# Optimization experiments

Measured on AMD Instinct MI355X. Metric: run time of the kernel, lower is better.

## Reference

```python
import jax, jax.numpy as jnp
from jax import lax
import numpy as np

B, T, I, H = 512, 512, 128, 256


def setup_inputs() -> dict:
    key = jax.random.key(0)
    ks = jax.random.split(key, 7)
    s = 1.0 / np.sqrt(H)  # pytorch-style init scale
    return {
        "x": jax.random.normal(ks[0], (B, T, I), dtype=jnp.float32),
        "h0": jax.random.normal(ks[1], (1, B, H), dtype=jnp.float32),
        "c0": jax.random.normal(ks[2], (1, B, H), dtype=jnp.float32),
        "w_ih": jax.random.normal(ks[3], (4 * H, I), dtype=jnp.float32) * s,
        "w_hh": jax.random.normal(ks[4], (4 * H, H), dtype=jnp.float32) * s,
        "b_ih": jax.random.normal(ks[5], (4 * H,), dtype=jnp.float32) * s,
        "b_hh": jax.random.normal(ks[6], (4 * H,), dtype=jnp.float32) * s,
    }


def reference(x, h0, c0, w_ih, w_hh, b_ih, b_hh):
    """Single-layer LSTM; returns final cell state c_n of shape [1, B, H].
    Gate row order in w_*/b_* is PyTorch's (i, f, g, o) blocks of H."""
    h = h0[0]  # [B, H]
    c = c0[0]  # [B, H]
    # Precompute input contribution for all timesteps: [T, B, 4H]
    xg = jnp.einsum('bti,gi->tbg', x, w_ih) + (b_ih + b_hh)

    def step(carry, xg_t):
        h, c = carry
        g = xg_t + h @ w_hh.T  # [B, 4H]
        gi, gf, gg, go = jnp.split(g, 4, axis=-1)
        c_new = jax.nn.sigmoid(gf) * c + jax.nn.sigmoid(gi) * jnp.tanh(gg)
        h_new = jax.nn.sigmoid(go) * jnp.tanh(c_new)
        return (h_new, c_new), None

    (h_T, c_T), _ = lax.scan(step, (h, c), xg)
    return c_T[None]  # [1, B, H]
```

## Files before the change

kernel.cpp:

```cpp
#include <hip/hip_runtime.h>
#include <hip/hip_bf16.h>
#include <hip/hip_fp16.h>


typedef __attribute__((ext_vector_type(4))) float f32x4;
typedef __attribute__((ext_vector_type(8))) _Float16 f16x8;
typedef __attribute__((ext_vector_type(4))) unsigned int u32x4;
typedef __attribute__((ext_vector_type(4))) int i32x4;

static __device__ __forceinline__ float h2f(unsigned short u) {
  return (float)__builtin_bit_cast(_Float16, u);
}
static __device__ __forceinline__ unsigned short f2h(float f) {
  return __builtin_bit_cast(unsigned short, (_Float16)f);
}
static __device__ __forceinline__ float fast_sigmoid(float x) {
  return __builtin_amdgcn_rcpf(1.0f + __builtin_amdgcn_exp2f(-1.44269504f * x));
}
static __device__ __forceinline__ float fast_tanh(float x) {
  return 1.0f - 2.0f * __builtin_amdgcn_rcpf(1.0f + __builtin_amdgcn_exp2f(2.88539008f * x));
}

__global__ void zero2(float* p) { if (threadIdx.x < 2) p[threadIdx.x] = 0.f; }

__global__ void absmax_red(const float* __restrict__ src, int n, float* __restrict__ out) {
  __shared__ float s[256];
  float m = 0.f;
  for (int i = blockIdx.x * 256 + threadIdx.x; i < n; i += gridDim.x * 256)
    m = fmaxf(m, fabsf(src[i]));
  s[threadIdx.x] = m; __syncthreads();
  for (int w = 128; w > 0; w >>= 1) {
    if (threadIdx.x < w) s[threadIdx.x] = fmaxf(s[threadIdx.x], s[threadIdx.x + w]);
    __syncthreads();
  }
  if (threadIdx.x == 0) atomicMax((int*)out, __float_as_int(s[0]));
}

__global__ void quant_w(const float* __restrict__ w, const float* __restrict__ scales,
                        signed char* __restrict__ wq, int n) {
  int i = blockIdx.x * 256 + threadIdx.x;
  if (i < n) {
    float inv = 127.0f / scales[0];
    int q = (int)rintf(w[i] * inv);
    q = max(-127, min(127, q));
    wq[i] = (signed char)q;
  }
}

__global__ void wperm_cast(const float* __restrict__ w, unsigned short* __restrict__ dst) {
  int i = (blockIdx.x * 256 + threadIdx.x) * 4;
  if (i < 131072) {
    int q = i >> 7, k = i & 127;
    int p = (q & 3) * 256 + (q >> 2);
    f32x4 v = *(const f32x4*)(w + p * 128 + k);
    ushort4 pk;
    pk.x = f2h(v[0]); pk.y = f2h(v[1]); pk.z = f2h(v[2]); pk.w = f2h(v[3]);
    *(ushort4*)(dst + i) = pk;
  }
}

__global__ void bias_perm(const float* __restrict__ bi, const float* __restrict__ bh,
                          float* __restrict__ bc) {
  int q = blockIdx.x * 256 + threadIdx.x;
  int p = (q & 3) * 256 + (q >> 2);
  bc[q] = bi[p] + bh[p];
}

__global__ void state_init(const float* __restrict__ h0, const float* __restrict__ c0,
                           const float* __restrict__ scales,
                           signed char* __restrict__ hst, float* __restrict__ cst) {
  int i = blockIdx.x * 256 + threadIdx.x;
  float inv = 127.0f / scales[1];
  int q = (int)rintf(h0[i] * inv);
  q = max(-127, min(127, q));
  hst[i] = (signed char)q;
  cst[i] = c0[i];
}

__global__ __launch_bounds__(256) void xgemm(
    const float* __restrict__ x, const unsigned short* __restrict__ wih,
    const float* __restrict__ bconv,
    unsigned short* __restrict__ xg, int t0, int tclog) {
  __shared__ unsigned short Ash[128 * 128];
  __shared__ unsigned short Bsh[128 * 128];

  const int tid  = threadIdx.x;
  const int lane = tid & 63;
  const int wv   = tid >> 6;
  const int c16  = lane & 15;
  const int gq   = lane >> 4;
  const long m0  = (long)blockIdx.x * 128;
  const int tcm  = (1 << tclog) - 1;

#pragma unroll
  for (int i = 0; i < 16; ++i) {
    int fidx = (i * 256 + tid) * 4;
    int row = fidx >> 7, k = fidx & 127;
    long cr = m0 + row;
    long b  = cr >> tclog;
    long tl = cr & tcm;
    f32x4 v = *(const f32x4*)(x + ((size_t)b * 512 + t0 + tl) * 128 + k);
    ushort4 pk;
    pk.x = f2h(v[0]); pk.y = f2h(v[1]); pk.z = f2h(v[2]); pk.w = f2h(v[3]);
    int byte = (row * 256 + k * 2) ^ ((row & 7) << 4);
    *(ushort4*)((char*)Ash + byte) = pk;
  }

  const int mh = (wv >> 1) * 64;
  const int nh = (wv & 1) * 64;

  for (int nc = 0; nc < 8; ++nc) {
    __syncthreads();
    {
      const char* wb = (const char*)(wih + nc * 128 * 128);
#pragma unroll
      for (int i = 0; i < 8; ++i) {
        int idx16 = i * 256 + tid;
        int row = idx16 >> 4, ch = idx16 & 15;
        int srcoff = row * 256 + ((ch * 16) ^ ((row & 7) << 4));
        u32x4 v = *(const u32x4*)(wb + srcoff);
        *(u32x4*)((char*)Bsh + idx16 * 16) = v;
      }
    }
    __syncthreads();

    float bias_v[4];
#pragma unroll
    for (int nt = 0; nt < 4; ++nt)
      bias_v[nt] = bconv[nc * 128 + nh + nt * 16 + c16];

    f16x8 af[4][4], bfr[4][4];
#pragma unroll
    for (int sm = 0; sm < 4; ++sm)
#pragma unroll
      for (int kt = 0; kt < 4; ++kt) {
        int m = mh + sm * 16 + c16;
        int byte = (m * 256 + (kt * 32 + gq * 8) * 2) ^ ((m & 7) << 4);
        af[sm][kt] = __builtin_bit_cast(f16x8, *(const u32x4*)((const char*)Ash + byte));
      }
#pragma unroll
    for (int nt = 0; nt < 4; ++nt)
#pragma unroll
      for (int kt = 0; kt < 4; ++kt) {
        int n = nh + nt * 16 + c16;
        int byte = (n * 256 + (kt * 32 + gq * 8) * 2) ^ ((n & 7) << 4);
        bfr[nt][kt] = __builtin_bit_cast(f16x8, *(const u32x4*)((const char*)Bsh + byte));
      }

    f32x4 acc[4][4];
#pragma unroll
    for (int sm = 0; sm < 4; ++sm)
#pragma unroll
      for (int nt = 0; nt < 4; ++nt) { f32x4 z = {0.f, 0.f, 0.f, 0.f}; acc[sm][nt] = z; }
#pragma unroll
    for (int sm = 0; sm < 4; ++sm)
#pragma unroll
      for (int nt = 0; nt < 4; ++nt)
#pragma unroll
        for (int kt = 0; kt < 4; ++kt)
          acc[sm][nt] = __builtin_amdgcn_mfma_f32_16x16x32_f16(af[sm][kt], bfr[nt][kt], acc[sm][nt], 0, 0, 0);

#pragma unroll
    for (int sm = 0; sm < 4; ++sm)
#pragma unroll
      for (int nt = 0; nt < 4; ++nt) {
        long row = m0 + mh + sm * 16 + gq * 4;
        int gcol = nc * 128 + nh + nt * 16 + c16;
#pragma unroll
        for (int r = 0; r < 4; ++r)
          xg[(size_t)(row + r) * 1024 + gcol] = f2h(acc[sm][nt][r] + bias_v[nt]);
      }
  }
}

__global__ __launch_bounds__(512)
__attribute__((amdgpu_waves_per_eu(2, 2)))
void fused_chunk(
    const unsigned short* __restrict__ xgc, const signed char* __restrict__ wq,
    const float* __restrict__ scales, signed char* __restrict__ hst,
    float* __restrict__ cst, float* __restrict__ out, int Tc, int first, int last,
    const float* __restrict__ x, const unsigned short* __restrict__ wih,
    const float* __restrict__ bconv, unsigned short* __restrict__ xgn,
    int t0n, int tclog, int do_x) {
  __shared__ char smem[65536];

  const int tid  = threadIdx.x;
  const int lane = tid & 63;
  const int wv   = tid >> 6;
  const int c16  = lane & 15;
  const int gq   = lane >> 4;

  if (blockIdx.x < 128) {
    signed char (*hb)[1280] = (signed char (*)[1280])smem;
    const int b0 = blockIdx.x * 4;

    const int col = wv * 32 + c16;
    float cv0 = cst[(b0 + gq) * 256 + col];
    float cv1 = cst[(b0 + gq) * 256 + col + 16];

    const float sw   = scales[0] * (1.0f / 127.0f);
    const float facR = sw * (1.0f / 127.0f);
    const float fac0 = first ? sw * (scales[1] * (1.0f / 127.0f)) : facR;

    i32x4 wf[8][4];
#pragma unroll
    for (int nt = 0; nt < 8; ++nt)
#pragma unroll
      for (int kt = 0; kt < 4; ++kt) {
        int n = (nt >> 1) * 256 + wv * 32 + (nt & 1) * 16 + c16;
        wf[nt][kt] = *(const i32x4*)(wq + n * 256 + kt * 64 + gq * 16);
      }
#pragma unroll
    for (int nt = 0; nt < 8; ++nt)
#pragma unroll
      for (int kt = 0; kt < 4; ++kt)
        asm volatile("" : "+v"(wf[nt][kt]));
    asm volatile("" ::: "memory");

    for (int i = tid; i < 1024; i += 512) {
      int row = i >> 8, cc = i & 255;
      hb[0][row * 320 + cc] = hst[(b0 + row) * 256 + cc];
    }

    const char* pxp = (const char*)(xgc + ((size_t)(b0 + gq) * Tc) * 1024 + col * 4);
    ushort4 px0 = *(const ushort4*)pxp;
    ushort4 px1 = *(const ushort4*)(pxp + 128);
    pxp += 2048;

    const bool mrow = (c16 & 3) == 0;
    const int  hrow = c16 >> 2;
    i32x4 af[4];
#pragma unroll
    for (int kt = 0; kt < 4; ++kt) { i32x4 z = {0, 0, 0, 0}; af[kt] = z; }
    const i32x4 zacc = {0, 0, 0, 0};
    int q0 = 0, q1 = 0;

    __syncthreads();

    for (int tt = 0; tt < Tc; ++tt) {
      const int cur = tt & 1;

      if (mrow) {
        const signed char* hp = &hb[cur][hrow * 320 + gq * 16];
        af[0] = *(const i32x4*)(hp);
        af[1] = *(const i32x4*)(hp + 64);
        af[2] = *(const i32x4*)(hp + 128);
        af[3] = *(const i32x4*)(hp + 192);
      }

      ushort4 pn0 = *(const ushort4*)pxp;
      ushort4 pn1 = *(const ushort4*)(pxp + 128);
      pxp += 2048;

      i32x4 acc[8];
#pragma unroll
      for (int ne = 0; ne < 4; ++ne)
        acc[2 * ne] = __builtin_amdgcn_mfma_i32_16x16x64_i8(af[0], wf[2 * ne][0], zacc, 0, 0, 0);
#pragma unroll
      for (int kt = 1; kt < 4; ++kt)
#pragma unroll
        for (int ne = 0; ne < 4; ++ne)
          acc[2 * ne] = __builtin_amdgcn_mfma_i32_16x16x64_i8(af[kt], wf[2 * ne][kt], acc[2 * ne], 0, 0, 0);
#pragma unroll
      for (int ne = 0; ne < 4; ++ne)
        acc[2 * ne + 1] = __builtin_amdgcn_mfma_i32_16x16x64_i8(af[0], wf[2 * ne + 1][0], zacc, 0, 0, 0);
#pragma unroll
      for (int kt = 1; kt < 4; ++kt)
#pragma unroll
        for (int ne = 0; ne < 4; ++ne)
          acc[2 * ne + 1] = __builtin_amdgcn_mfma_i32_16x16x64_i8(af[kt], wf[2 * ne + 1][kt], acc[2 * ne + 1], 0, 0, 0);

      const float fac = (tt == 0) ? fac0 : facR;

      {
        float gi = __builtin_fmaf((float)acc[0][0], fac, h2f(px0.x));
        float gf = __builtin_fmaf((float)acc[2][0], fac, h2f(px0.y));
        float gg = __builtin_fmaf((float)acc[4][0], fac, h2f(px0.z));
        float go = __builtin_fmaf((float)acc[6][0], fac, h2f(px0.w));
        cv0 = fast_sigmoid(gf) * cv0 + fast_sigmoid(gi) * fast_tanh(gg);
        float hn = fast_sigmoid(go) * fast_tanh(cv0);
        q0 = (int)rintf(hn * 127.0f);
        hb[cur ^ 1][gq * 320 + col] = (signed char)q0;
      }
      {
        float gi = __builtin_fmaf((float)acc[1][0], fac, h2f(px1.x));
        float gf = __builtin_fmaf((float)acc[3][0], fac, h2f(px1.y));
        float gg = __builtin_fmaf((float)acc[5][0], fac, h2f(px1.z));
        float go = __builtin_fmaf((float)acc[7][0], fac, h2f(px1.w));
        cv1 = fast_sigmoid(gf) * cv1 + fast_sigmoid(gi) * fast_tanh(gg);
        float hn = fast_sigmoid(go) * fast_tanh(cv1);
        q1 = (int)rintf(hn * 127.0f);
        hb[cur ^ 1][gq * 320 + col + 16] = (signed char)q1;
      }

      px0 = pn0; px1 = pn1;
      __syncthreads();
    }

    cst[(b0 + gq) * 256 + col]      = cv0;
    cst[(b0 + gq) * 256 + col + 16] = cv1;
    hst[(b0 + gq) * 256 + col]      = (signed char)q0;
    hst[(b0 + gq) * 256 + col + 16] = (signed char)q1;
    if (last) {
      out[(b0 + gq) * 256 + col]      = cv0;
      out[(b0 + gq) * 256 + col + 16] = cv1;
    }
  } else if (do_x) {
    unsigned short* Ash = (unsigned short*)smem;
    unsigned short* Bsh = (unsigned short*)(smem + 32768);
    const int tcm    = (1 << tclog) - 1;
    const int ntiles = Tc << 2;
    const int wm = wv >> 2, wn = wv & 3;
    const int mh = wm * 64, nh = wn * 32;

    for (int rt = (int)blockIdx.x - 128; rt < ntiles; rt += 128) {
      const long m0 = (long)rt * 128;
      __syncthreads();

#pragma unroll
      for (int i = 0; i < 8; ++i) {
        int fidx = (i * 512 + tid) * 4;
        int row = fidx >> 7, k = fidx & 127;
        long cr = m0 + row;
        long b  = cr >> tclog;
        long tl = cr & tcm;
        f32x4 v = *(const f32x4*)(x + ((size_t)b * 512 + t0n + tl) * 128 + k);
        ushort4 pk;
        pk.x = f2h(v[0]); pk.y = f2h(v[1]); pk.z = f2h(v[2]); pk.w = f2h(v[3]);
        int byte = (row * 256 + k * 2) ^ ((row & 7) << 4);
        *(ushort4*)((char*)Ash + byte) = pk;
      }

      for (int nc = 0; nc < 8; ++nc) {
        __syncthreads();
        {
          const char* wb = (const char*)(wih + nc * 128 * 128);
#pragma unroll
          for (int i = 0; i < 4; ++i) {
            int idx16 = i * 512 + tid;
            int row = idx16 >> 4, ch = idx16 & 15;
            int srcoff = row * 256 + ((ch * 16) ^ ((row & 7) << 4));
            u32x4 v = *(const u32x4*)(wb + srcoff);
            *(u32x4*)((char*)Bsh + idx16 * 16) = v;
          }
        }
        __syncthreads();

        float bias_v[2];
#pragma unroll
        for (int nt = 0; nt < 2; ++nt)
          bias_v[nt] = bconv[nc * 128 + nh + nt * 16 + c16];

        f16x8 af[4][4], bfr[2][4];
#pragma unroll
        for (int sm = 0; sm < 4; ++sm)
#pragma unroll
          for (int kt = 0; kt < 4; ++kt) {
            int m = mh + sm * 16 + c16;
            int byte = (m * 256 + (kt * 32 + gq * 8) * 2) ^ ((m & 7) << 4);
            af[sm][kt] = __builtin_bit_cast(f16x8, *(const u32x4*)((const char*)Ash + byte));
          }
#pragma unroll
        for (int nt = 0; nt < 2; ++nt)
#pragma unroll
          for (int kt = 0; kt < 4; ++kt) {
            int n = nh + nt * 16 + c16;
            int byte = (n * 256 + (kt * 32 + gq * 8) * 2) ^ ((n & 7) << 4);
            bfr[nt][kt] = __builtin_bit_cast(f16x8, *(const u32x4*)((const char*)Bsh + byte));
          }

        f32x4 acc[4][2];
#pragma unroll
        for (int sm = 0; sm < 4; ++sm)
#pragma unroll
          for (int nt = 0; nt < 2; ++nt) { f32x4 z = {0.f, 0.f, 0.f, 0.f}; acc[sm][nt] = z; }
#pragma unroll
        for (int sm = 0; sm < 4; ++sm)
#pragma unroll
          for (int nt = 0; nt < 2; ++nt)
#pragma unroll
            for (int kt = 0; kt < 4; ++kt)
              acc[sm][nt] = __builtin_amdgcn_mfma_f32_16x16x32_f16(af[sm][kt], bfr[nt][kt], acc[sm][nt], 0, 0, 0);

#pragma unroll
        for (int sm = 0; sm < 4; ++sm)
#pragma unroll
          for (int nt = 0; nt < 2; ++nt) {
            long row = m0 + mh + sm * 16 + gq * 4;
            int gcol = nc * 128 + nh + nt * 16 + c16;
#pragma unroll
            for (int r = 0; r < 4; ++r)
              xgn[(size_t)(row + r) * 1024 + gcol] = f2h(acc[sm][nt][r] + bias_v[nt]);
          }
      }
    }
  }
}

extern "C" void kernel_launch(void* const* d_in, const int* in_sizes, int n_in,
                              void* d_out, int out_size, void* d_ws, size_t ws_size,
                              hipStream_t stream) {
  const float* x   = (const float*)d_in[0];
  const float* h0  = (const float*)d_in[1];
  const float* c0  = (const float*)d_in[2];
  const float* wih = (const float*)d_in[3];
  const float* whh = (const float*)d_in[4];
  const float* bih = (const float*)d_in[5];
  const float* bhh = (const float*)d_in[6];
  float* out = (float*)d_out;

  const size_t fixed = 262144u  + 262144u  + 131072u
                     + 524288u  + 4096u  + 256u ;
  int tc = 512;
  while (tc > 4 && 2u * (size_t)512 * tc * 2048 + fixed > ws_size) tc >>= 1;
  int tclog = 31 - __builtin_clz((unsigned)tc);
  size_t bufsz = (size_t)512 * tc * 2048;

  char* ws = (char*)d_ws;
  unsigned short* xgb0  = (unsigned short*)ws;
  unsigned short* xgb1  = (unsigned short*)(ws + bufsz);
  size_t off = 2u * bufsz;
  unsigned short* wih_h = (unsigned short*)(ws + off);  off += 262144u;
  signed char*    wqb   = (signed char*)(ws + off);     off += 262144u;
  signed char*    hst   = (signed char*)(ws + off);     off += 131072u;
  float*          cst   = (float*)(ws + off);           off += 524288u;
  float*          bcv   = (float*)(ws + off);           off += 4096u;
  float*          scl   = (float*)(ws + off);

  zero2<<<1, 64, 0, stream>>>(scl);
  absmax_red<<<128, 256, 0, stream>>>(whh, 262144, scl + 0);
  absmax_red<<<64, 256, 0, stream>>>(h0, 131072, scl + 1);
  wperm_cast<<<128, 256, 0, stream>>>(wih, wih_h);
  bias_perm<<<4, 256, 0, stream>>>(bih, bhh, bcv);
  quant_w<<<1024, 256, 0, stream>>>(whh, scl, wqb, 262144);
  state_init<<<512, 256, 0, stream>>>(h0, c0, scl, hst, cst);

  xgemm<<<4 * tc, 256, 0, stream>>>(x, wih_h, bcv, xgb0, 0, tclog);

  int NC = 512 / tc;
  for (int c = 0; c < NC; ++c) {
    unsigned short* cur = (c & 1) ? xgb1 : xgb0;
    unsigned short* nxt = (c & 1) ? xgb0 : xgb1;
    int do_x = (c + 1 < NC) ? 1 : 0;
    fused_chunk<<<256, 512, 0, stream>>>(
        cur, wqb, scl, hst, cst, out, tc, (c == 0) ? 1 : 0, (c == NC - 1) ? 1 : 0,
        x, wih_h, bcv, nxt, (c + 1) * tc, tclog, do_x);
  }
}
```

Measured before the change: 541.8 us.

## Merge setup kernels into two prep launches and shrink the time chunk

Replaces seven small setup kernels (zero, two absmax reductions, cast/permute, bias, quantize, state init) with two launches. The first writes per-block partial maxima and does the weight cast and bias permutation; the second reduces those partials and quantizes weights and state. This removes the atomics and the zeroing kernel. It also lowers the starting time-chunk size from 512 to 128, so the recurrence runs in four chunks with the next chunk's input GEMM overlapped, at the cost of more launches.

```diff
diff --git a/kernel.cpp b/kernel.cpp
--- a/kernel.cpp
+++ b/kernel.cpp
@@ -21,60 +21,83 @@
   return 1.0f - 2.0f * __builtin_amdgcn_rcpf(1.0f + __builtin_amdgcn_exp2f(2.88539008f * x));
 }
 
-__global__ void zero2(float* p) { if (threadIdx.x < 2) p[threadIdx.x] = 0.f; }
-
-__global__ void absmax_red(const float* __restrict__ src, int n, float* __restrict__ out) {
-  __shared__ float s[256];
-  float m = 0.f;
-  for (int i = blockIdx.x * 256 + threadIdx.x; i < n; i += gridDim.x * 256)
-    m = fmaxf(m, fabsf(src[i]));
-  s[threadIdx.x] = m; __syncthreads();
-  for (int w = 128; w > 0; w >>= 1) {
-    if (threadIdx.x < w) s[threadIdx.x] = fmaxf(s[threadIdx.x], s[threadIdx.x + w]);
-    __syncthreads();
-  }
-  if (threadIdx.x == 0) atomicMax((int*)out, __float_as_int(s[0]));
-}
-
-__global__ void quant_w(const float* __restrict__ w, const float* __restrict__ scales,
-                        signed char* __restrict__ wq, int n) {
-  int i = blockIdx.x * 256 + threadIdx.x;
-  if (i < n) {
-    float inv = 127.0f / scales[0];
-    int q = (int)rintf(w[i] * inv);
-    q = max(-127, min(127, q));
-    wq[i] = (signed char)q;
-  }
-}
-
-__global__ void wperm_cast(const float* __restrict__ w, unsigned short* __restrict__ dst) {
-  int i = (blockIdx.x * 256 + threadIdx.x) * 4;
-  if (i < 131072) {
+__global__ __launch_bounds__(256) void prep1(
+    const float* __restrict__ whh, const float* __restrict__ h0,
+    const float* __restrict__ wih, const float* __restrict__ bih,
+    const float* __restrict__ bhh,
+    float* __restrict__ scl, unsigned short* __restrict__ wih_h,
+    float* __restrict__ bcv) {
+  const int b = blockIdx.x, tid = threadIdx.x;
+  if (b < 192) {
+    __shared__ float s[256];
+    const float* src = (b < 128) ? whh : h0;
+    int base = (b < 128) ? b * 2048 : (b - 128) * 2048;
+    float m = 0.f;
+#pragma unroll
+    for (int i = 0; i < 8; ++i) m = fmaxf(m, fabsf(src[base + i * 256 + tid]));
+    s[tid] = m; __syncthreads();
+    for (int w = 128; w > 0; w >>= 1) {
+      if (tid < w) s[tid] = fmaxf(s[tid], s[tid + w]);
+      __syncthreads();
+    }
+    if (tid == 0) scl[8 + b] = s[0];
+  } else {
+    int i = ((b - 192) * 256 + tid) * 4;
     int q = i >> 7, k = i & 127;
     int p = (q & 3) * 256 + (q >> 2);
-    f32x4 v = *(const f32x4*)(w + p * 128 + k);
+    f32x4 v = *(const f32x4*)(wih + p * 128 + k);
     ushort4 pk;
     pk.x = f2h(v[0]); pk.y = f2h(v[1]); pk.z = f2h(v[2]); pk.w = f2h(v[3]);
-    *(ushort4*)(dst + i) = pk;
-  }
-}
-
-__global__ void bias_perm(const float* __restrict__ bi, const float* __restrict__ bh,
-                          float* __restrict__ bc) {
-  int q = blockIdx.x * 256 + threadIdx.x;
-  int p = (q & 3) * 256 + (q >> 2);
-  bc[q] = bi[p] + bh[p];
-}
-
-__global__ void state_init(const float* __restrict__ h0, const float* __restrict__ c0,
-                           const float* __restrict__ scales,
-                           signed char* __restrict__ hst, float* __restrict__ cst) {
-  int i = blockIdx.x * 256 + threadIdx.x;
-  float inv = 127.0f / scales[1];
-  int q = (int)rintf(h0[i] * inv);
-  q = max(-127, min(127, q));
-  hst[i] = (signed char)q;
-  cst[i] = c0[i];
+    *(ushort4*)(wih_h + i) = pk;
+    if (b == 192) {
+      for (int q2 = tid; q2 < 1024; q2 += 256) {
+        int p2 = (q2 & 3) * 256 + (q2 >> 2);
+        bcv[q2] = bih[p2] + bhh[p2];
+      }
+    }
+  }
+}
+
+__global__ __launch_bounds__(256) void prep2(
+    const float* __restrict__ whh, const float* __restrict__ h0,
+    const float* __restrict__ c0, float* __restrict__ scl,
+    signed char* __restrict__ wq, signed char* __restrict__ hst,
+    float* __restrict__ cst) {
+  __shared__ float s[256];
+  const int b = blockIdx.x, tid = threadIdx.x;
+  float v = (tid < 128) ? scl[8 + tid] : 0.f;
+  s[tid] = v; __syncthreads();
+  for (int w = 128; w > 0; w >>= 1) {
+    if (tid < w) s[tid] = fmaxf(s[tid], s[tid + w]);
+    __syncthreads();
+  }
+  float sw = s[0]; __syncthreads();
+  v = (tid < 64) ? scl[136 + tid] : 0.f;
+  s[tid] = v; __syncthreads();
+  for (int w = 128; w > 0; w >>= 1) {
+    if (tid < w) s[tid] = fmaxf(s[tid], s[tid + w]);
+    __syncthreads();
+  }
+  float sh = s[0];
+  if (b == 0 && tid == 0) { scl[0] = sw; scl[1] = sh; }
+
+  const float invw = 127.0f / sw;
+  int base = b * 1024;
+#pragma unroll
+  for (int i = 0; i < 4; ++i) {
+    int idx = base + i * 256 + tid;
+    int q = (int)rintf(whh[idx] * invw);
+    wq[idx] = (signed char)max(-127, min(127, q));
+  }
+  const float invh = 127.0f / sh;
+  int sb = b * 512;
+#pragma unroll
+  for (int i = 0; i < 2; ++i) {
+    int idx = sb + i * 256 + tid;
+    int q = (int)rintf(h0[idx] * invh);
+    hst[idx] = (signed char)max(-127, min(127, q));
+    cst[idx] = c0[idx];
+  }
 }
 
 __global__ __launch_bounds__(256) void xgemm(
@@ -410,8 +433,8 @@
   float* out = (float*)d_out;
 
   const size_t fixed = 262144u  + 262144u  + 131072u
-                     + 524288u  + 4096u  + 256u ;
-  int tc = 512;
+                     + 524288u  + 4096u  + 1024u ;
+  int tc = 128;
   while (tc > 4 && 2u * (size_t)512 * tc * 2048 + fixed > ws_size) tc >>= 1;
   int tclog = 31 - __builtin_clz((unsigned)tc);
   size_t bufsz = (size_t)512 * tc * 2048;
@@ -427,13 +450,8 @@
   float*          bcv   = (float*)(ws + off);           off += 4096u;
   float*          scl   = (float*)(ws + off);
 
-  zero2<<<1, 64, 0, stream>>>(scl);
-  absmax_red<<<128, 256, 0, stream>>>(whh, 262144, scl + 0);
-  absmax_red<<<64, 256, 0, stream>>>(h0, 131072, scl + 1);
-  wperm_cast<<<128, 256, 0, stream>>>(wih, wih_h);
-  bias_perm<<<4, 256, 0, stream>>>(bih, bhh, bcv);
-  quant_w<<<1024, 256, 0, stream>>>(whh, scl, wqb, 262144);
-  state_init<<<512, 256, 0, stream>>>(h0, c0, scl, hst, cst);
+  prep1<<<320, 256, 0, stream>>>(whh, h0, wih, bih, bhh, scl, wih_h, bcv);
+  prep2<<<256, 256, 0, stream>>>(whh, h0, c0, scl, wqb, hst, cst);
 
   xgemm<<<4 * tc, 256, 0, stream>>>(x, wih_h, bcv, xgb0, 0, tclog);
 
```

Result: no change. 531.3 us (-1.9%).
